# Kernel tuning notes

Hardware: AMD Instinct MI355X
Metric: run time of the kernel (lower is better)

The kernel has to match this reference:

```python
import jax, jax.numpy as jnp
import numpy as np

N_NODE = 100000
N_EDGE = 1600000
D_NODE = 32
D_EDGE = 16
D_OUT = 32
D_IN = 2 * D_NODE + D_EDGE  # 80
D_HID = 2 * D_IN            # 160


def setup_inputs() -> dict:
    key = jax.random.key(0)
    ks = jax.random.split(key, 6)
    nodes = jax.random.normal(ks[0], (N_NODE, D_NODE), dtype=jnp.float32)
    edges = jax.random.normal(ks[1], (N_EDGE, D_EDGE), dtype=jnp.float32)
    senders = jax.random.randint(ks[2], (N_EDGE,), 0, N_NODE, dtype=jnp.int64 if jax.config.jax_enable_x64 else jnp.int32)
    receivers = jax.random.randint(ks[3], (N_EDGE,), 0, N_NODE, dtype=jnp.int64 if jax.config.jax_enable_x64 else jnp.int32)
    # Linear params (fan-in scaled like torch's default init scale)
    W1 = jax.random.normal(ks[4], (D_IN, D_HID), dtype=jnp.float32) / np.sqrt(D_IN)
    b1 = jnp.zeros((D_HID,), dtype=jnp.float32)
    W2 = jax.random.normal(ks[5], (D_HID, D_OUT), dtype=jnp.float32) / np.sqrt(D_HID)
    b2 = jnp.zeros((D_OUT,), dtype=jnp.float32)
    return {"nodes": nodes, "edges": edges, "senders": senders,
            "receivers": receivers, "W1": W1, "b1": b1, "W2": W2, "b2": b2}


def reference(nodes, edges, senders, receivers, W1, b1, W2, b2):
    # gather sender/receiver node features and concat with edge features: [E, 2*d_node+d_edge]
    feats = jnp.concatenate([nodes[senders], nodes[receivers], edges], axis=1)
    h = jax.nn.sigmoid(feats @ W1 + b1)   # [E, 2*d_in]
    new_edges = h @ W2 + b2               # [E, d_edge_out]
    return new_edges
```

## Files before the change

kernel.cpp:

```cpp
#include <hip/hip_runtime.h>

#define NEDGE  1600000
#define NPT    (NEDGE / 16)
#define GRID   2500
#define NIT    (NPT / GRID)
#define NNODE  100000
#define NB_OFF 32768
#define WS_BYTES (65536 + NNODE * 32 * 2)

typedef float f32x4  __attribute__((ext_vector_type(4)));
typedef short short8 __attribute__((ext_vector_type(8)));

static __device__ __forceinline__ ushort f2bf(float f) {
  uint u = __builtin_bit_cast(uint, f);
  return (ushort)((u + 0x7FFFu + ((u >> 16) & 1u)) >> 16);
}
static __device__ __forceinline__ uint cvt_pk(float lo, float hi) {
  uint r; asm("v_cvt_pk_bf16_f32 %0, %1, %2" : "=v"(r) : "v"(lo), "v"(hi)); return r;
}
static __device__ __forceinline__ float vexp2(float x) {
  float r; asm("v_exp_f32 %0, %1" : "=v"(r) : "v"(x)); return r;
}
static __device__ __forceinline__ float vrcp(float x) {
  float r; asm("v_rcp_f32 %0, %1" : "=v"(r) : "v"(x)); return r;
}
static __device__ __forceinline__ short8 pack8(float4 a, float4 b) {
  uint4 u;
  u.x = cvt_pk(a.x, a.y); u.y = cvt_pk(a.z, a.w);
  u.z = cvt_pk(b.x, b.y); u.w = cvt_pk(b.z, b.w);
  return __builtin_bit_cast(short8, u);
}

__global__ void prep_frags(const float* __restrict__ W1, const float* __restrict__ b1,
                           const float* __restrict__ W2, ushort* __restrict__ ws) {
  const int idx = blockIdx.x * 256 + threadIdx.x;
  if (idx >= 20480) return;
  const int frag = idx >> 9;
  const int lane = (idx >> 3) & 63;
  const int j    = idx & 7;
  const int g = lane >> 4, c = lane & 15;
  ushort v;
  if (frag < 30) {
    const int wh = frag / 15, rem = frag % 15, mt = rem / 3, kt = rem % 3;
    const int k   = kt * 32 + g * 8 + j;
    const int hid = 32 * mt + 8 * (c >> 2) + 4 * wh + (c & 3);
    const float s = -1.44269504088896f;
    const float val = (k < 80) ? W1[k * 160 + hid] * s
                               : (k == 80 ? b1[hid] * s : 0.0f);
    v = f2bf(val);
  } else {
    const int f2 = frag - 30, wh = f2 / 5, kt = f2 % 5;
    const int k = kt * 32 + g * 8 + j;
    v = f2bf(W2[k * 32 + 16 * wh + c]);
  }
  ws[idx] = v;
}

__global__ void prep_nodes(const float* __restrict__ nodes, ushort* __restrict__ nb) {
  const int idx = blockIdx.x * 256 + threadIdx.x;
  if (idx >= NNODE * 4) return;
  const float4 a = ((const float4*)nodes)[idx * 2];
  const float4 b = ((const float4*)nodes)[idx * 2 + 1];
  *(short8*)(nb + (size_t)idx * 8) = pack8(a, b);
}

template <bool USE_WS>
__global__ __launch_bounds__(128) void edge_mlp(
    const float* __restrict__ nodes, const float* __restrict__ edges,
    const int* __restrict__ senders, const int* __restrict__ receivers,
    const float* __restrict__ W1, const float* __restrict__ b1,
    const float* __restrict__ W2, const float* __restrict__ b2,
    float* __restrict__ out, const ushort* __restrict__ ws)
{
  __shared__ uint2 X[2][2][5][64];

  const int lane = threadIdx.x & 63;
  const int wh   = threadIdx.x >> 6;
  const int g    = lane >> 4;
  const int c    = lane & 15;
  const ushort* nb = USE_WS ? (ws + NB_OFF) : nullptr;

  short8 w1f[5][3];
  short8 w2f[5];
  if constexpr (USE_WS) {
#pragma unroll
    for (int mt = 0; mt < 5; ++mt)
#pragma unroll
      for (int kt = 0; kt < 3; ++kt)
        w1f[mt][kt] = *(const short8*)(ws + ((wh * 15 + mt * 3 + kt) * 64 + lane) * 8);
#pragma unroll
    for (int kt = 0; kt < 5; ++kt)
      w2f[kt] = *(const short8*)(ws + ((30 + wh * 5 + kt) * 64 + lane) * 8);
  } else {
    const float s = -1.44269504088896f;
    const int hidb = 8 * (c >> 2) + 4 * wh + (c & 3);
#pragma unroll
    for (int mt = 0; mt < 5; ++mt)
#pragma unroll
      for (int kt = 0; kt < 3; ++kt) {
        const int hid = 32 * mt + hidb;
        uint d[4];
#pragma unroll
        for (int dw = 0; dw < 4; ++dw) {
          const int k0 = kt * 32 + g * 8 + dw * 2, k1 = k0 + 1;
          const float f0 = (k0 < 80) ? W1[k0 * 160 + hid] * s : (k0 == 80 ? b1[hid] * s : 0.f);
          const float f1 = (k1 < 80) ? W1[k1 * 160 + hid] * s : (k1 == 80 ? b1[hid] * s : 0.f);
          d[dw] = (uint)f2bf(f0) | ((uint)f2bf(f1) << 16);
        }
        w1f[mt][kt] = __builtin_bit_cast(short8, make_uint4(d[0], d[1], d[2], d[3]));
      }
#pragma unroll
    for (int kt = 0; kt < 5; ++kt) {
      uint d[4];
#pragma unroll
      for (int dw = 0; dw < 4; ++dw) {
        const int k = kt * 32 + g * 8 + dw * 2;
        d[dw] = (uint)f2bf(W2[k * 32 + wh * 16 + c]) |
                ((uint)f2bf(W2[(k + 1) * 32 + wh * 16 + c]) << 16);
      }
      w2f[kt] = __builtin_bit_cast(short8, make_uint4(d[0], d[1], d[2], d[3]));
    }
  }
  const float4 b2v = *(const float4*)(b2 + wh * 16 + g * 4);
  const uint   cE0 = (g == 2) ? 0x3F80u : 0u;

  int t = blockIdx.x;
  int e = t * 16 + c;
  short8 bfS_p, bfR_p;
  float4 sn0, sn1, rn0, rn1;
  float4 ee0, ee1;
  {
    const int si = senders[e], ri = receivers[e];
    if constexpr (USE_WS) {
      bfS_p = *(const short8*)(nb + (size_t)si * 32 + g * 8);
      bfR_p = *(const short8*)(nb + (size_t)ri * 32 + g * 8);
    } else {
      const float* sp = nodes + (size_t)si * 32 + g * 8;
      sn0 = *(const float4*)sp;  sn1 = *(const float4*)(sp + 4);
      const float* rp = nodes + (size_t)ri * 32 + g * 8;
      rn0 = *(const float4*)rp;  rn1 = *(const float4*)(rp + 4);
    }
    const float* ep = edges + (size_t)e * 16 + (g & 1) * 8;
    ee0 = *(const float4*)ep;  ee1 = *(const float4*)(ep + 4);
  }
  int e1 = (t + GRID) * 16 + c;
  int si1 = senders[e1], ri1 = receivers[e1];

  for (int i = 0; i < NIT; ++i) {
    const int buf = i & 1;

    uint4 ue;
    ue.x = (g < 2) ? cvt_pk(ee0.x, ee0.y) : cE0;
    ue.y = (g < 2) ? cvt_pk(ee0.z, ee0.w) : 0u;
    ue.z = (g < 2) ? cvt_pk(ee1.x, ee1.y) : 0u;
    ue.w = (g < 2) ? cvt_pk(ee1.z, ee1.w) : 0u;
    const short8 bfE = __builtin_bit_cast(short8, ue);
    short8 bfS, bfR;
    if constexpr (USE_WS) { bfS = bfS_p;            bfR = bfR_p; }
    else                  { bfS = pack8(sn0, sn1);  bfR = pack8(rn0, rn1); }

    f32x4 acc[5];
#pragma unroll
    for (int mt = 0; mt < 5; ++mt) acc[mt] = (f32x4){0.f, 0.f, 0.f, 0.f};
#pragma unroll
    for (int mt = 0; mt < 5; ++mt)
      acc[mt] = __builtin_amdgcn_mfma_f32_16x16x32_bf16(w1f[mt][0], bfS, acc[mt], 0, 0, 0);
#pragma unroll
    for (int mt = 0; mt < 5; ++mt)
      acc[mt] = __builtin_amdgcn_mfma_f32_16x16x32_bf16(w1f[mt][1], bfR, acc[mt], 0, 0, 0);
#pragma unroll
    for (int mt = 0; mt < 5; ++mt)
      acc[mt] = __builtin_amdgcn_mfma_f32_16x16x32_bf16(w1f[mt][2], bfE, acc[mt], 0, 0, 0);

    {
      int tn = t + GRID; if (tn >= NPT) tn = t;
      const int en = tn * 16 + c;
      const float* epn = edges + (size_t)en * 16 + (g & 1) * 8;
      ee0 = *(const float4*)epn;  ee1 = *(const float4*)(epn + 4);
      if constexpr (USE_WS) {
        bfS_p = *(const short8*)(nb + (size_t)si1 * 32 + g * 8);
        bfR_p = *(const short8*)(nb + (size_t)ri1 * 32 + g * 8);
      } else {
        const float* spn = nodes + (size_t)si1 * 32 + g * 8;
        sn0 = *(const float4*)spn;  sn1 = *(const float4*)(spn + 4);
        const float* rpn = nodes + (size_t)ri1 * 32 + g * 8;
        rn0 = *(const float4*)rpn;  rn1 = *(const float4*)(rpn + 4);
      }
      int t2 = t + 2 * GRID; if (t2 >= NPT) t2 = tn;
      const int e2 = t2 * 16 + c;
      si1 = senders[e2];  ri1 = receivers[e2];
    }

    uint pkA[5], pkB[5];
#pragma unroll
    for (int mt = 0; mt < 5; ++mt) {
      const float h0 = vrcp(1.0f + vexp2(acc[mt][0]));
      const float h1 = vrcp(1.0f + vexp2(acc[mt][1]));
      const float h2 = vrcp(1.0f + vexp2(acc[mt][2]));
      const float h3 = vrcp(1.0f + vexp2(acc[mt][3]));
      pkA[mt] = cvt_pk(h0, h1);
      pkB[mt] = cvt_pk(h2, h3);
    }

#pragma unroll
    for (int kt = 0; kt < 5; ++kt) X[wh][buf][kt][lane] = make_uint2(pkA[kt], pkB[kt]);
    asm volatile("s_waitcnt lgkmcnt(0)\n\ts_barrier" ::: "memory");
    uint2 q[5];
#pragma unroll
    for (int kt = 0; kt < 5; ++kt) q[kt] = X[wh ^ 1][buf][kt][lane];

    f32x4 oa = (f32x4){b2v.x, b2v.y, b2v.z, b2v.w};
    f32x4 ob = (f32x4){0.f, 0.f, 0.f, 0.f};
    if (wh == 0) {
#pragma unroll
      for (int kt = 0; kt < 5; ++kt) {
        const short8 bb = __builtin_bit_cast(short8,
            make_uint4(pkA[kt], pkB[kt], q[kt].x, q[kt].y));
        if (kt & 1) ob = __builtin_amdgcn_mfma_f32_16x16x32_bf16(w2f[kt], bb, ob, 0, 0, 0);
        else        oa = __builtin_amdgcn_mfma_f32_16x16x32_bf16(w2f[kt], bb, oa, 0, 0, 0);
      }
    } else {
#pragma unroll
      for (int kt = 0; kt < 5; ++kt) {
        const short8 bb = __builtin_bit_cast(short8,
            make_uint4(q[kt].x, q[kt].y, pkA[kt], pkB[kt]));
        if (kt & 1) ob = __builtin_amdgcn_mfma_f32_16x16x32_bf16(w2f[kt], bb, ob, 0, 0, 0);
        else        oa = __builtin_amdgcn_mfma_f32_16x16x32_bf16(w2f[kt], bb, oa, 0, 0, 0);
      }
    }
    const f32x4 o = oa + ob;

    float4 st; st.x = o[0]; st.y = o[1]; st.z = o[2]; st.w = o[3];
    *(float4*)(out + (size_t)e * 32 + wh * 16 + g * 4) = st;

    t += GRID;
    e = t * 16 + c;
  }
}

extern "C" void kernel_launch(void* const* d_in, const int* in_sizes, int n_in,
                              void* d_out, int out_size, void* d_ws, size_t ws_size,
                              hipStream_t stream) {
  const float* nodes     = (const float*)d_in[0];
  const float* edges     = (const float*)d_in[1];
  const int*   senders   = (const int*)d_in[2];
  const int*   receivers = (const int*)d_in[3];
  const float* W1        = (const float*)d_in[4];
  const float* b1        = (const float*)d_in[5];
  const float* W2        = (const float*)d_in[6];
  const float* b2        = (const float*)d_in[7];
  float* out = (float*)d_out;

  if (ws_size >= (size_t)WS_BYTES) {
    ushort* ws = (ushort*)d_ws;
    prep_frags<<<80, 256, 0, stream>>>(W1, b1, W2, ws);
    prep_nodes<<<(NNODE * 4 + 255) / 256, 256, 0, stream>>>(nodes, ws + NB_OFF);
    edge_mlp<true><<<GRID, 128, 0, stream>>>(nodes, edges, senders, receivers,
                                             W1, b1, W2, b2, out, ws);
  } else {
    edge_mlp<false><<<GRID, 128, 0, stream>>>(nodes, edges, senders, receivers,
                                              W1, b1, W2, b2, out, nullptr);
  }
}
```

Measured before the change: 157.5 us.

## Double grid size and simplify MFMA accumulator chains in edge MLP kernel

Raises the persistent grid from 2500 to 5000 blocks, so each block runs half as many iterations while more blocks are resident. The first-layer MFMA now takes a zero constant as its accumulator instead of zero-initialised registers. The second layer drops the two interleaved accumulators and their final add in favour of one chain seeded with the bias. The single chain removes a vector add and some registers, but each MFMA must now wait on the previous one's result.

```diff
diff --git a/kernel.cpp b/kernel.cpp
--- a/kernel.cpp
+++ b/kernel.cpp
@@ -2,7 +2,7 @@
 
 #define NEDGE  1600000
 #define NPT    (NEDGE / 16)
-#define GRID   2500
+#define GRID   5000
 #define NIT    (NPT / GRID)
 #define NNODE  100000
 #define NB_OFF 32768
@@ -122,7 +122,9 @@
     }
   }
   const float4 b2v = *(const float4*)(b2 + wh * 16 + g * 4);
-  const uint   cE0 = (g == 2) ? 0x3F80u : 0u;
+  const f32x4 b2c = (f32x4){b2v.x, b2v.y, b2v.z, b2v.w};
+  const f32x4 z4  = (f32x4){0.f, 0.f, 0.f, 0.f};
+  const uint  cE0 = (g == 2) ? 0x3F80u : 0u;
 
   int t = blockIdx.x;
   int e = t * 16 + c;
@@ -161,10 +163,8 @@
 
     f32x4 acc[5];
 #pragma unroll
-    for (int mt = 0; mt < 5; ++mt) acc[mt] = (f32x4){0.f, 0.f, 0.f, 0.f};
-#pragma unroll
-    for (int mt = 0; mt < 5; ++mt)
-      acc[mt] = __builtin_amdgcn_mfma_f32_16x16x32_bf16(w1f[mt][0], bfS, acc[mt], 0, 0, 0);
+    for (int mt = 0; mt < 5; ++mt)
+      acc[mt] = __builtin_amdgcn_mfma_f32_16x16x32_bf16(w1f[mt][0], bfS, z4, 0, 0, 0);
 #pragma unroll
     for (int mt = 0; mt < 5; ++mt)
       acc[mt] = __builtin_amdgcn_mfma_f32_16x16x32_bf16(w1f[mt][1], bfR, acc[mt], 0, 0, 0);
@@ -209,26 +209,22 @@
 #pragma unroll
     for (int kt = 0; kt < 5; ++kt) q[kt] = X[wh ^ 1][buf][kt][lane];
 
-    f32x4 oa = (f32x4){b2v.x, b2v.y, b2v.z, b2v.w};
-    f32x4 ob = (f32x4){0.f, 0.f, 0.f, 0.f};
+    f32x4 o;
     if (wh == 0) {
-#pragma unroll
-      for (int kt = 0; kt < 5; ++kt) {
-        const short8 bb = __builtin_bit_cast(short8,
-            make_uint4(pkA[kt], pkB[kt], q[kt].x, q[kt].y));
-        if (kt & 1) ob = __builtin_amdgcn_mfma_f32_16x16x32_bf16(w2f[kt], bb, ob, 0, 0, 0);
-        else        oa = __builtin_amdgcn_mfma_f32_16x16x32_bf16(w2f[kt], bb, oa, 0, 0, 0);
-      }
+      o = __builtin_amdgcn_mfma_f32_16x16x32_bf16(w2f[0],
+            __builtin_bit_cast(short8, make_uint4(pkA[0], pkB[0], q[0].x, q[0].y)), b2c, 0, 0, 0);
+#pragma unroll
+      for (int kt = 1; kt < 5; ++kt)
+        o = __builtin_amdgcn_mfma_f32_16x16x32_bf16(w2f[kt],
+              __builtin_bit_cast(short8, make_uint4(pkA[kt], pkB[kt], q[kt].x, q[kt].y)), o, 0, 0, 0);
     } else {
-#pragma unroll
-      for (int kt = 0; kt < 5; ++kt) {
-        const short8 bb = __builtin_bit_cast(short8,
-            make_uint4(q[kt].x, q[kt].y, pkA[kt], pkB[kt]));
-        if (kt & 1) ob = __builtin_amdgcn_mfma_f32_16x16x32_bf16(w2f[kt], bb, ob, 0, 0, 0);
-        else        oa = __builtin_amdgcn_mfma_f32_16x16x32_bf16(w2f[kt], bb, oa, 0, 0, 0);
-      }
-    }
-    const f32x4 o = oa + ob;
+      o = __builtin_amdgcn_mfma_f32_16x16x32_bf16(w2f[0],
+            __builtin_bit_cast(short8, make_uint4(q[0].x, q[0].y, pkA[0], pkB[0])), b2c, 0, 0, 0);
+#pragma unroll
+      for (int kt = 1; kt < 5; ++kt)
+        o = __builtin_amdgcn_mfma_f32_16x16x32_bf16(w2f[kt],
+              __builtin_bit_cast(short8, make_uint4(q[kt].x, q[kt].y, pkA[kt], pkB[kt])), o, 0, 0, 0);
+    }
 
     float4 st; st.x = o[0]; st.y = o[1]; st.z = o[2]; st.w = o[3];
     *(float4*)(out + (size_t)e * 32 + wh * 16 + g * 4) = st;
```

Measured after the change: 162.7 us. 1.03x slower.
